# Optimization experiments

Hardware: AMD Instinct MI355X
Metric: run time of the kernel (lower is better)

The kernel has to match this reference:

```python
import jax, jax.numpy as jnp
import numpy as np

EPS = 1e-12  # F.normalize default eps


def _sage_conv(x, src, dst, num_nodes, W_l, W_r, b):
    # mean-aggregate neighbor features: for each dst node, mean over x[src]
    agg = jax.ops.segment_sum(x[src], dst, num_segments=num_nodes)  # [N, d_in]
    cnt = jax.ops.segment_sum(jnp.ones((src.shape[0],), x.dtype), dst,
                              num_segments=num_nodes)
    mean = agg / jnp.maximum(cnt, 1.0)[:, None]
    # PyG SAGEConv: lin_l(aggregated) + bias + lin_r(root)
    return mean @ W_l + b + x @ W_r


def setup_inputs() -> dict:
    key = jax.random.key(0)
    ks = jax.random.split(key, 10)
    N, E, F_in = 50000, 400000, 128
    x = jax.random.normal(ks[0], (N, F_in), dtype=jnp.float32)
    edge_index = jax.random.randint(ks[1], (2, E), 0, N, dtype=jnp.int64)

    def lin(k, din, dout):
        s = 1.0 / np.sqrt(din)
        return jax.random.uniform(k, (din, dout), jnp.float32, -s, s)

    params = {
        "W1_l": lin(ks[2], F_in, 2048), "W1_r": lin(ks[3], F_in, 2048),
        "b1": jnp.zeros((2048,), jnp.float32),
        "W2_l": lin(ks[4], 2048, 2048), "W2_r": lin(ks[5], 2048, 2048),
        "b2": jnp.zeros((2048,), jnp.float32),
        "W3_l": lin(ks[6], 2048, 1024), "W3_r": lin(ks[7], 2048, 1024),
        "b3": jnp.zeros((1024,), jnp.float32),
    }
    return {"x": x, "unused": 0, "edge_index": edge_index, **params}


def reference(x, unused, edge_index,
              W1_l, W1_r, b1, W2_l, W2_r, b2, W3_l, W3_r, b3):
    del unused
    N = x.shape[0]
    src, dst = edge_index[0], edge_index[1]
    h = jax.nn.relu(_sage_conv(x, src, dst, N, W1_l, W1_r, b1))
    h = jax.nn.relu(_sage_conv(h, src, dst, N, W2_l, W2_r, b2))
    h = jax.nn.relu(_sage_conv(h, src, dst, N, W3_l, W3_r, b3))
    # F.normalize(dim=1): x / max(||x||_2, eps)
    norm = jnp.linalg.norm(h, axis=1, keepdims=True)
    return h / jnp.maximum(norm, EPS)
```

## Files before the change

### kernel.cpp

```cpp
#include <hip/hip_runtime.h>
#include <stdint.h>

#define NN 50000
#define EE 400000

typedef unsigned short u16;
typedef __attribute__((ext_vector_type(8))) short bf16x8;
typedef __attribute__((ext_vector_type(4))) float f32x4;
typedef __attribute__((address_space(3))) uint32_t lds_u32_t;
typedef __attribute__((address_space(1))) uint32_t glob_u32_t;

__device__ inline float bf2f(u16 u) {
  union { uint32_t i; float f; } x; x.i = ((uint32_t)u) << 16; return x.f;
}
__device__ inline u16 f2bf(float f) {
  union { float f; uint32_t i; } x; x.f = f;
  x.i += 0x7fffu + ((x.i >> 16) & 1u);
  return (u16)(x.i >> 16);
}
__device__ inline void gload_lds16(const void* g, void* l) {
  __builtin_amdgcn_global_load_lds((const glob_u32_t*)g, (lds_u32_t*)l, 16, 0, 0);
}

__global__ void detect_i64(const int* __restrict__ e, int* __restrict__ flag) {
  __shared__ int sh[256];
  int t = threadIdx.x;
  int v = 0;
  for (int i = t; i < 4096; i += 256) v |= e[2 * i + 1];
  sh[t] = v; __syncthreads();
  for (int s = 128; s > 0; s >>= 1) { if (t < s) sh[t] |= sh[t + s]; __syncthreads(); }
  if (t == 0) flag[0] = (sh[0] == 0) ? 1 : 0;
}

__global__ void conv_count(const int* __restrict__ e, const int* __restrict__ flag,
                           int* __restrict__ src, int* __restrict__ dst,
                           int* __restrict__ cnt) {
  int i = blockIdx.x * 256 + threadIdx.x;
  if (i >= EE) return;
  int s, d;
  if (flag[0]) { s = e[2 * i]; d = e[2 * (EE + i)]; }
  else         { s = e[i];     d = e[EE + i]; }
  src[i] = s; dst[i] = d;
  atomicAdd(&cnt[d], 1);
}

__global__ void assign_offs(const int* __restrict__ cnt, int* __restrict__ offs,
                            int* __restrict__ cursor, int* __restrict__ gcur) {
  int i = blockIdx.x * 256 + threadIdx.x;
  if (i >= NN) return;
  int c = cnt[i];
  int b = atomicAdd(gcur, c);
  offs[i] = b; cursor[i] = b;
}

__global__ void fill_buckets(const int* __restrict__ src, const int* __restrict__ dst,
                             int* __restrict__ cursor, int* __restrict__ bucket) {
  int i = blockIdx.x * 256 + threadIdx.x;
  if (i >= EE) return;
  int p = atomicAdd(&cursor[dst[i]], 1);
  bucket[p] = src[i];
}

__global__ void cvt_bf16(const float* __restrict__ in, u16* __restrict__ out, int n4) {
  int i = blockIdx.x * 256 + threadIdx.x;
  if (i >= n4) return;
  float4 v = ((const float4*)in)[i];
  u16 o[4] = { f2bf(v.x), f2bf(v.y), f2bf(v.z), f2bf(v.w) };
  uint2 pack;
  pack.x = (uint32_t)o[0] | ((uint32_t)o[1] << 16);
  pack.y = (uint32_t)o[2] | ((uint32_t)o[3] << 16);
  ((uint2*)out)[i] = pack;
}

__global__ void transposeW(const float* __restrict__ W, u16* __restrict__ Wt,
                           int K, int Nc) {
  __shared__ float tile[32][33];
  int n0 = blockIdx.x * 32, k0 = blockIdx.y * 32;
  int tx = threadIdx.x, ty = threadIdx.y;
  #pragma unroll
  for (int i = 0; i < 4; ++i)
    tile[ty + i * 8][tx] = W[(size_t)(k0 + ty + i * 8) * Nc + n0 + tx];
  __syncthreads();
  #pragma unroll
  for (int i = 0; i < 4; ++i)
    Wt[(size_t)(n0 + ty + i * 8) * K + k0 + tx] = f2bf(tile[tx][ty + i * 8]);
}

template<int D>
__global__ void agg_mean(const u16* __restrict__ h, const int* __restrict__ offs,
                         const int* __restrict__ cnt, const int* __restrict__ bucket,
                         u16* __restrict__ outp) {
  int node = blockIdx.x;
  int t = threadIdx.x;
  int base = t * 8;
  if (base >= D) return;
  int start = offs[node];
  int c = cnt[node];
  float acc[8];
  #pragma unroll
  for (int i = 0; i < 8; ++i) acc[i] = 0.f;
  for (int j = 0; j < c; ++j) {
    int s = bucket[start + j];
    uint4 q = *(const uint4*)(h + (size_t)s * D + base);
    acc[0] += bf2f((u16)(q.x & 0xffff)); acc[1] += bf2f((u16)(q.x >> 16));
    acc[2] += bf2f((u16)(q.y & 0xffff)); acc[3] += bf2f((u16)(q.y >> 16));
    acc[4] += bf2f((u16)(q.z & 0xffff)); acc[5] += bf2f((u16)(q.z >> 16));
    acc[6] += bf2f((u16)(q.w & 0xffff)); acc[7] += bf2f((u16)(q.w >> 16));
  }
  float inv = 1.0f / fmaxf((float)c, 1.0f);
  uint4 o;
  o.x = (uint32_t)f2bf(acc[0] * inv) | ((uint32_t)f2bf(acc[1] * inv) << 16);
  o.y = (uint32_t)f2bf(acc[2] * inv) | ((uint32_t)f2bf(acc[3] * inv) << 16);
  o.z = (uint32_t)f2bf(acc[4] * inv) | ((uint32_t)f2bf(acc[5] * inv) << 16);
  o.w = (uint32_t)f2bf(acc[6] * inv) | ((uint32_t)f2bf(acc[7] * inv) << 16);
  *(uint4*)(outp + (size_t)node * D + base) = o;
}

__global__ void agg_add_norm(const u16* __restrict__ Y, const int* __restrict__ offs,
                             const int* __restrict__ cnt, const int* __restrict__ bucket,
                             const float* __restrict__ b3, float* __restrict__ outp) {
  int node = blockIdx.x;
  int t = threadIdx.x;
  int base = t * 4;
  int start = offs[node];
  int c = cnt[node];
  float acc[4] = {0.f, 0.f, 0.f, 0.f};
  for (int j = 0; j < c; ++j) {
    int s = bucket[start + j];
    uint2 q = *(const uint2*)(Y + (size_t)s * 2048 + base);
    acc[0] += bf2f((u16)(q.x & 0xffff)); acc[1] += bf2f((u16)(q.x >> 16));
    acc[2] += bf2f((u16)(q.y & 0xffff)); acc[3] += bf2f((u16)(q.y >> 16));
  }
  float inv = 1.0f / fmaxf((float)c, 1.0f);
  uint2 qr = *(const uint2*)(Y + (size_t)node * 2048 + 1024 + base);
  float yr[4] = { bf2f((u16)(qr.x & 0xffff)), bf2f((u16)(qr.x >> 16)),
                  bf2f((u16)(qr.y & 0xffff)), bf2f((u16)(qr.y >> 16)) };
  float4 bv = *(const float4*)(b3 + base);
  float v[4];
  v[0] = fmaxf(acc[0] * inv + yr[0] + bv.x, 0.f);
  v[1] = fmaxf(acc[1] * inv + yr[1] + bv.y, 0.f);
  v[2] = fmaxf(acc[2] * inv + yr[2] + bv.z, 0.f);
  v[3] = fmaxf(acc[3] * inv + yr[3] + bv.w, 0.f);
  float ss = v[0] * v[0] + v[1] * v[1] + v[2] * v[2] + v[3] * v[3];
  #pragma unroll
  for (int off = 32; off > 0; off >>= 1) ss += __shfl_down(ss, off);
  __shared__ float sw[4];
  int lane = t & 63, w = t >> 6;
  if (lane == 0) sw[w] = ss;
  __syncthreads();
  float total = sw[0] + sw[1] + sw[2] + sw[3];
  float scale = 1.0f / fmaxf(sqrtf(total), 1e-12f);
  float4 o = { v[0] * scale, v[1] * scale, v[2] * scale, v[3] * scale };
  *(float4*)(outp + (size_t)node * 1024 + base) = o;
}


template<int K>
__device__ inline void stage_half(char* ldsX, const u16* __restrict__ G, int grow0,
                                  int k0, int h, int wave, int lrow8, int slot8,
                                  int clampR) {
  #pragma unroll
  for (int j = 0; j < 2; ++j) {
    const int lrow = h * 128 + j * 64 + wave * 8;
    int gr = grow0 + lrow + lrow8;
    gr = gr < clampR ? gr : clampR - 1;
    gload_lds16(G + (size_t)gr * K + k0 + slot8, ldsX + lrow * 128);
  }
}

#define LOAD_A(MH)                                                              \
  _Pragma("unroll") for (int mf = 0; mf < 4; ++mf) {                            \
    af[mf][0] = *(const bf16x8*)(cA + ((MH) * 128 + mf * 16) * 128 + kc0);      \
    af[mf][1] = *(const bf16x8*)(cA + ((MH) * 128 + mf * 16) * 128 + kc1);      \
  }
#define LOAD_B(DST, NH)                                                         \
  _Pragma("unroll") for (int nf = 0; nf < 2; ++nf) {                            \
    DST[nf][0] = *(const bf16x8*)(cB + ((NH) * 128 + nf * 16) * 128 + kc0);     \
    DST[nf][1] = *(const bf16x8*)(cB + ((NH) * 128 + nf * 16) * 128 + kc1);     \
  }
#define QUAD(MH, BREG, NH)                                                      \
  _Pragma("unroll") for (int mf = 0; mf < 4; ++mf)                              \
  _Pragma("unroll") for (int nf = 0; nf < 2; ++nf) {                            \
    acc[(MH)*4+mf][(NH)*2+nf] = __builtin_amdgcn_mfma_f32_16x16x32_bf16(        \
        af[mf][0], BREG[nf][0], acc[(MH)*4+mf][(NH)*2+nf], 0, 0, 0);            \
    acc[(MH)*4+mf][(NH)*2+nf] = __builtin_amdgcn_mfma_f32_16x16x32_bf16(        \
        af[mf][1], BREG[nf][1], acc[(MH)*4+mf][(NH)*2+nf], 0, 0, 0);            \
  }

template<int K, bool DUAL, bool EPI, bool OUT_F32>
__global__ __launch_bounds__(512, 2)
void gemm2src(const u16* __restrict__ A1, const u16* __restrict__ A2,
              const u16* __restrict__ B1t, const u16* __restrict__ B2t,
              const float* __restrict__ bias, void* __restrict__ Cout,
              int M, int Nc, int tilesN) {
  __shared__ __align__(16) char lds[131072];
  constexpr int NTp = K / 64;
  constexpr int NT = DUAL ? 2 * NTp : NTp;

  const int nwg = gridDim.x;
  const int bid = blockIdx.x;
  const int wg = (bid & 7) * (nwg >> 3) + (bid >> 3);
  const int bx = wg % tilesN, by = wg / tilesN;
  const int rowBase = by * 256, colBase = bx * 256;

  const int tid = threadIdx.x;
  const int lane = tid & 63;
  const int wave = tid >> 6;
  const int wm = wave >> 2, wn = wave & 3;
  const int r = lane & 15, kg = lane >> 4;
  const int sw = (r & 7) << 4;
  const int kc0 = (kg * 16) ^ sw;
  const int kc1 = (64 + kg * 16) ^ sw;
  const int slot8 = ((lane & 7) ^ ((lane >> 3) & 7)) * 8;
  const int lrow8 = lane >> 3;

  char* const pA0 = lds + (wm * 64 + r) * 128;
  char* const pB0 = lds + 32768 + (wn * 32 + r) * 128;

  f32x4 acc[8][4];
  #pragma unroll
  for (int m = 0; m < 8; ++m)
    #pragma unroll
    for (int n = 0; n < 4; ++n) acc[m][n] = (f32x4){0.f, 0.f, 0.f, 0.f};

  bf16x8 af[4][2], b0[2][2], b1[2][2];

  stage_half<K>(lds,         A1,  rowBase, 0, 0, wave, lrow8, slot8, M);
  stage_half<K>(lds + 32768, B1t, colBase, 0, 0, wave, lrow8, slot8, Nc);
  stage_half<K>(lds + 32768, B1t, colBase, 0, 1, wave, lrow8, slot8, Nc);
  stage_half<K>(lds,         A1,  rowBase, 0, 1, wave, lrow8, slot8, M);
  asm volatile("s_waitcnt vmcnt(4)" ::: "memory");
  __builtin_amdgcn_s_barrier();

  for (int t = 0; t < NT; ++t) {
    const int cur = t & 1;
    const char* cA = pA0 + cur * 65536;
    const char* cB = pB0 + cur * 65536;
    char* nA = lds + (cur ^ 1) * 65536;
    char* nB = nA + 32768;
    const int vt = (t + 1 < NT) ? t + 1 : NT - 1;
    const u16* sA; const u16* sB; int sk0;
    if (DUAL && vt >= NTp) { sA = A2; sB = B2t; sk0 = (vt - NTp) * 64; }
    else                   { sA = A1; sB = B1t; sk0 = vt * 64; }

    LOAD_A(0); LOAD_B(b0, 0);
    stage_half<K>(nA, sA, rowBase, sk0, 0, wave, lrow8, slot8, M);
    __builtin_amdgcn_s_barrier();
    asm volatile("s_waitcnt lgkmcnt(0)" ::: "memory");
    __builtin_amdgcn_s_setprio(1);
    QUAD(0, b0, 0);
    __builtin_amdgcn_s_setprio(0);
    asm volatile("s_waitcnt vmcnt(4)" ::: "memory");
    __builtin_amdgcn_s_barrier();

    LOAD_B(b1, 1);
    stage_half<K>(nB, sB, colBase, sk0, 0, wave, lrow8, slot8, Nc);
    __builtin_amdgcn_s_barrier();
    asm volatile("s_waitcnt lgkmcnt(0)" ::: "memory");
    __builtin_amdgcn_s_setprio(1);
    QUAD(0, b1, 1);
    __builtin_amdgcn_s_setprio(0);
    asm volatile("s_waitcnt vmcnt(4)" ::: "memory");
    __builtin_amdgcn_s_barrier();

    LOAD_A(1);
    stage_half<K>(nB, sB, colBase, sk0, 1, wave, lrow8, slot8, Nc);
    __builtin_amdgcn_s_barrier();
    asm volatile("s_waitcnt lgkmcnt(0)" ::: "memory");
    __builtin_amdgcn_s_setprio(1);
    QUAD(1, b1, 1);
    __builtin_amdgcn_s_setprio(0);
    __builtin_amdgcn_s_barrier();

    stage_half<K>(nA, sA, rowBase, sk0, 1, wave, lrow8, slot8, M);
    __builtin_amdgcn_s_barrier();
    __builtin_amdgcn_s_setprio(1);
    QUAD(1, b0, 0);
    __builtin_amdgcn_s_setprio(0);
    asm volatile("s_waitcnt vmcnt(4)" ::: "memory");
    __builtin_amdgcn_s_barrier();
  }

  asm volatile("s_waitcnt vmcnt(0)" ::: "memory");

  const int q = lane >> 4;
  #pragma unroll
  for (int m = 0; m < 8; ++m) {
    int row = rowBase + (m >> 2) * 128 + wm * 64 + (m & 3) * 16 + q * 4;
    #pragma unroll
    for (int n = 0; n < 4; ++n) {
      int col = colBase + (n >> 1) * 128 + wn * 32 + (n & 1) * 16 + r;
      float bv = EPI ? bias[col] : 0.f;
      #pragma unroll
      for (int reg = 0; reg < 4; ++reg) {
        if (row + reg < M) {
          float v = acc[m][n][reg];
          if constexpr (EPI) v = fmaxf(v + bv, 0.f);
          if constexpr (OUT_F32)
            ((float*)Cout)[(size_t)(row + reg) * Nc + col] = v;
          else
            ((u16*)Cout)[(size_t)(row + reg) * Nc + col] = f2bf(v);
        }
      }
    }
  }
}

extern "C" void kernel_launch(void* const* d_in, const int* in_sizes, int n_in,
                              void* d_out, int out_size, void* d_ws, size_t ws_size,
                              hipStream_t stream) {
  const float* x   = (const float*)d_in[0];
  const int*   eix = (const int*)d_in[2];
  const float* W1l = (const float*)d_in[3];
  const float* W1r = (const float*)d_in[4];
  const float* b1  = (const float*)d_in[5];
  const float* W2l = (const float*)d_in[6];
  const float* W2r = (const float*)d_in[7];
  const float* b2  = (const float*)d_in[8];
  const float* W3l = (const float*)d_in[9];
  const float* W3r = (const float*)d_in[10];
  const float* b3  = (const float*)d_in[11];

  char* ws = (char*)d_ws;
  size_t off = 0;
  auto alloc = [&](size_t bytes) -> char* {
    char* p = ws + off;
    off += (bytes + 255) & ~(size_t)255;
    return p;
  };
  int* flag   = (int*)alloc(4);
  int* gcur   = (int*)alloc(4);
  int* srcA   = (int*)alloc((size_t)EE * 4);
  int* dstA   = (int*)alloc((size_t)EE * 4);
  int* bucket = (int*)alloc((size_t)EE * 4);
  int* cnt    = (int*)alloc((size_t)NN * 4);
  int* offs   = (int*)alloc((size_t)NN * 4);
  int* cursor = (int*)alloc((size_t)NN * 4);
  u16* xb     = (u16*)alloc((size_t)NN * 128 * 2);
  u16* mean1  = (u16*)alloc((size_t)NN * 128 * 2);
  u16* W1lT   = (u16*)alloc((size_t)2048 * 128 * 2);
  u16* W1rT   = (u16*)alloc((size_t)2048 * 128 * 2);
  u16* W2lT   = (u16*)alloc((size_t)2048 * 2048 * 2);
  u16* W2rT   = (u16*)alloc((size_t)2048 * 2048 * 2);
  u16* W3lT   = (u16*)alloc((size_t)1024 * 2048 * 2);
  u16* W3rT   = (u16*)alloc((size_t)1024 * 2048 * 2);
  u16* bufA   = (u16*)alloc((size_t)NN * 2048 * 2);
  u16* bufB   = (u16*)alloc((size_t)NN * 2048 * 2);
  u16* mean2  = (u16*)d_out;

  detect_i64<<<1, 256, 0, stream>>>(eix, flag);
  hipMemsetAsync(cnt, 0, (size_t)NN * 4, stream);
  hipMemsetAsync(gcur, 0, 4, stream);
  conv_count<<<(EE + 255) / 256, 256, 0, stream>>>(eix, flag, srcA, dstA, cnt);
  assign_offs<<<(NN + 255) / 256, 256, 0, stream>>>(cnt, offs, cursor, gcur);
  fill_buckets<<<(EE + 255) / 256, 256, 0, stream>>>(srcA, dstA, cursor, bucket);

  cvt_bf16<<<(NN * 128 / 4 + 255) / 256, 256, 0, stream>>>(x, xb, NN * 128 / 4);
  transposeW<<<dim3(2048 / 32, 128 / 32), dim3(32, 8), 0, stream>>>(W1l, W1lT, 128, 2048);
  transposeW<<<dim3(2048 / 32, 128 / 32), dim3(32, 8), 0, stream>>>(W1r, W1rT, 128, 2048);
  transposeW<<<dim3(2048 / 32, 2048 / 32), dim3(32, 8), 0, stream>>>(W2l, W2lT, 2048, 2048);
  transposeW<<<dim3(2048 / 32, 2048 / 32), dim3(32, 8), 0, stream>>>(W2r, W2rT, 2048, 2048);
  transposeW<<<dim3(1024 / 32, 2048 / 32), dim3(32, 8), 0, stream>>>(W3l, W3lT, 2048, 1024);
  transposeW<<<dim3(1024 / 32, 2048 / 32), dim3(32, 8), 0, stream>>>(W3r, W3rT, 2048, 1024);

  const int tilesM = (NN + 255) / 256;

  agg_mean<128><<<NN, 64, 0, stream>>>(xb, offs, cnt, bucket, mean1);
  gemm2src<128, true, true, false><<<tilesM * 8, 512, 0, stream>>>(
      mean1, xb, W1lT, W1rT, b1, bufA, NN, 2048, 8);

  agg_mean<2048><<<NN, 256, 0, stream>>>(bufA, offs, cnt, bucket, mean2);
  gemm2src<2048, true, true, false><<<tilesM * 8, 512, 0, stream>>>(
      mean2, bufA, W2lT, W2rT, b2, bufB, NN, 2048, 8);

  gemm2src<2048, false, false, false><<<tilesM * 8, 512, 0, stream>>>(
      bufB, nullptr, W3lT, nullptr, nullptr, bufA, NN, 2048, 8);
  agg_add_norm<<<NN, 256, 0, stream>>>(bufA, offs, cnt, bucket, b3, (float*)d_out);
}
```

Baseline: 1.895 ms.

## Replace double-buffered pipelined GEMM mainloop with single-buffered load-wait-compute loop

The GEMM kernel drops its double-buffered LDS pipeline, which interleaved the next tile's global-to-LDS staging with MFMA work and used priority hints. Each K-step now stages the whole A and B tile into a single 64KB LDS buffer, waits for all loads, computes, then barriers. Halving LDS may allow more resident workgroups and simplifies synchronisation. In exchange, global load latency is no longer hidden behind compute within a workgroup.

```diff
diff --git a/kernel.cpp b/kernel.cpp
--- a/kernel.cpp
+++ b/kernel.cpp
@@ -170,13 +170,13 @@
 
 #define LOAD_A(MH)                                                              \
   _Pragma("unroll") for (int mf = 0; mf < 4; ++mf) {                            \
-    af[mf][0] = *(const bf16x8*)(cA + ((MH) * 128 + mf * 16) * 128 + kc0);      \
-    af[mf][1] = *(const bf16x8*)(cA + ((MH) * 128 + mf * 16) * 128 + kc1);      \
+    af[mf][0] = *(const bf16x8*)(pA0 + ((MH) * 128 + mf * 16) * 128 + kc0);     \
+    af[mf][1] = *(const bf16x8*)(pA0 + ((MH) * 128 + mf * 16) * 128 + kc1);     \
   }
 #define LOAD_B(DST, NH)                                                         \
   _Pragma("unroll") for (int nf = 0; nf < 2; ++nf) {                            \
-    DST[nf][0] = *(const bf16x8*)(cB + ((NH) * 128 + nf * 16) * 128 + kc0);     \
-    DST[nf][1] = *(const bf16x8*)(cB + ((NH) * 128 + nf * 16) * 128 + kc1);     \
+    DST[nf][0] = *(const bf16x8*)(pB0 + ((NH) * 128 + nf * 16) * 128 + kc0);    \
+    DST[nf][1] = *(const bf16x8*)(pB0 + ((NH) * 128 + nf * 16) * 128 + kc1);    \
   }
 #define QUAD(MH, BREG, NH)                                                      \
   _Pragma("unroll") for (int mf = 0; mf < 4; ++mf)                              \
@@ -189,11 +189,11 @@
 
 template<int K, bool DUAL, bool EPI, bool OUT_F32>
 __global__ __launch_bounds__(512, 2)
-void gemm2src(const u16* __restrict__ A1, const u16* __restrict__ A2,
-              const u16* __restrict__ B1t, const u16* __restrict__ B2t,
-              const float* __restrict__ bias, void* __restrict__ Cout,
-              int M, int Nc, int tilesN) {
-  __shared__ __align__(16) char lds[131072];
+void gemmSB(const u16* __restrict__ A1, const u16* __restrict__ A2,
+            const u16* __restrict__ B1t, const u16* __restrict__ B2t,
+            const float* __restrict__ bias, void* __restrict__ Cout,
+            int M, int Nc, int tilesN) {
+  __shared__ __align__(16) char lds[65536];
   constexpr int NTp = K / 64;
   constexpr int NT = DUAL ? 2 * NTp : NTp;
 
@@ -225,63 +225,27 @@
 
   bf16x8 af[4][2], b0[2][2], b1[2][2];
 
-  stage_half<K>(lds,         A1,  rowBase, 0, 0, wave, lrow8, slot8, M);
-  stage_half<K>(lds + 32768, B1t, colBase, 0, 0, wave, lrow8, slot8, Nc);
-  stage_half<K>(lds + 32768, B1t, colBase, 0, 1, wave, lrow8, slot8, Nc);
-  stage_half<K>(lds,         A1,  rowBase, 0, 1, wave, lrow8, slot8, M);
-  asm volatile("s_waitcnt vmcnt(4)" ::: "memory");
-  __builtin_amdgcn_s_barrier();
-
   for (int t = 0; t < NT; ++t) {
-    const int cur = t & 1;
-    const char* cA = pA0 + cur * 65536;
-    const char* cB = pB0 + cur * 65536;
-    char* nA = lds + (cur ^ 1) * 65536;
-    char* nB = nA + 32768;
-    const int vt = (t + 1 < NT) ? t + 1 : NT - 1;
-    const u16* sA; const u16* sB; int sk0;
-    if (DUAL && vt >= NTp) { sA = A2; sB = B2t; sk0 = (vt - NTp) * 64; }
-    else                   { sA = A1; sB = B1t; sk0 = vt * 64; }
+    const u16* sA; const u16* sB; int k0;
+    if (DUAL && t >= NTp) { sA = A2; sB = B2t; k0 = (t - NTp) * 64; }
+    else                  { sA = A1; sB = B1t; k0 = t * 64; }
+
+    stage_half<K>(lds,         sA, rowBase, k0, 0, wave, lrow8, slot8, M);
+    stage_half<K>(lds + 32768, sB, colBase, k0, 0, wave, lrow8, slot8, Nc);
+    stage_half<K>(lds + 32768, sB, colBase, k0, 1, wave, lrow8, slot8, Nc);
+    stage_half<K>(lds,         sA, rowBase, k0, 1, wave, lrow8, slot8, M);
+    asm volatile("s_waitcnt vmcnt(0)" ::: "memory");
+    __builtin_amdgcn_s_barrier();
 
     LOAD_A(0); LOAD_B(b0, 0);
-    stage_half<K>(nA, sA, rowBase, sk0, 0, wave, lrow8, slot8, M);
+    QUAD(0, b0, 0);
+    LOAD_B(b1, 1);
+    QUAD(0, b1, 1);
+    LOAD_A(1);
+    QUAD(1, b1, 1);
+    QUAD(1, b0, 0);
     __builtin_amdgcn_s_barrier();
-    asm volatile("s_waitcnt lgkmcnt(0)" ::: "memory");
-    __builtin_amdgcn_s_setprio(1);
-    QUAD(0, b0, 0);
-    __builtin_amdgcn_s_setprio(0);
-    asm volatile("s_waitcnt vmcnt(4)" ::: "memory");
-    __builtin_amdgcn_s_barrier();
-
-    LOAD_B(b1, 1);
-    stage_half<K>(nB, sB, colBase, sk0, 0, wave, lrow8, slot8, Nc);
-    __builtin_amdgcn_s_barrier();
-    asm volatile("s_waitcnt lgkmcnt(0)" ::: "memory");
-    __builtin_amdgcn_s_setprio(1);
-    QUAD(0, b1, 1);
-    __builtin_amdgcn_s_setprio(0);
-    asm volatile("s_waitcnt vmcnt(4)" ::: "memory");
-    __builtin_amdgcn_s_barrier();
-
-    LOAD_A(1);
-    stage_half<K>(nB, sB, colBase, sk0, 1, wave, lrow8, slot8, Nc);
-    __builtin_amdgcn_s_barrier();
-    asm volatile("s_waitcnt lgkmcnt(0)" ::: "memory");
-    __builtin_amdgcn_s_setprio(1);
-    QUAD(1, b1, 1);
-    __builtin_amdgcn_s_setprio(0);
-    __builtin_amdgcn_s_barrier();
-
-    stage_half<K>(nA, sA, rowBase, sk0, 1, wave, lrow8, slot8, M);
-    __builtin_amdgcn_s_barrier();
-    __builtin_amdgcn_s_setprio(1);
-    QUAD(1, b0, 0);
-    __builtin_amdgcn_s_setprio(0);
-    asm volatile("s_waitcnt vmcnt(4)" ::: "memory");
-    __builtin_amdgcn_s_barrier();
-  }
-
-  asm volatile("s_waitcnt vmcnt(0)" ::: "memory");
+  }
 
   const int q = lane >> 4;
   #pragma unroll
@@ -366,14 +330,14 @@
   const int tilesM = (NN + 255) / 256;
 
   agg_mean<128><<<NN, 64, 0, stream>>>(xb, offs, cnt, bucket, mean1);
-  gemm2src<128, true, true, false><<<tilesM * 8, 512, 0, stream>>>(
+  gemmSB<128, true, true, false><<<tilesM * 8, 512, 0, stream>>>(
       mean1, xb, W1lT, W1rT, b1, bufA, NN, 2048, 8);
 
   agg_mean<2048><<<NN, 256, 0, stream>>>(bufA, offs, cnt, bucket, mean2);
-  gemm2src<2048, true, true, false><<<tilesM * 8, 512, 0, stream>>>(
+  gemmSB<2048, true, true, false><<<tilesM * 8, 512, 0, stream>>>(
       mean2, bufA, W2lT, W2rT, b2, bufB, NN, 2048, 8);
 
-  gemm2src<2048, false, false, false><<<tilesM * 8, 512, 0, stream>>>(
+  gemmSB<2048, false, false, false><<<tilesM * 8, 512, 0, stream>>>(
       bufB, nullptr, W3lT, nullptr, nullptr, bufA, NN, 2048, 8);
   agg_add_norm<<<NN, 256, 0, stream>>>(bufA, offs, cnt, bucket, b3, (float*)d_out);
 }
```

New measurement: 2.510 ms. 32.5% more time.
